# Kernel optimization log

Measured on AMD Instinct MI355X. Metric: run time of the kernel, lower is better.

## Reference

```python
import jax, jax.numpy as jnp
import numpy as np

START, STOP = 3, 4  # tag_to_ix['<START>'], tag_to_ix['<STOP>']
NEG = -10000.0


def _lstm_dir(x, w_ih, w_hh, b_ih, b_hh, h0, c0, reverse):
    # x: [S, E]; PyTorch gate order i, f, g, o
    H2 = h0.shape[0]
    xg = x @ w_ih.T + b_ih + b_hh  # [S, 4*H2] precompute input part

    def step(carry, xt):
        h, c = carry
        g = xt + h @ w_hh.T
        i, f, gg, o = jnp.split(g, 4)
        i, f, o = jax.nn.sigmoid(i), jax.nn.sigmoid(f), jax.nn.sigmoid(o)
        c = f * c + i * jnp.tanh(gg)
        h = o * jnp.tanh(c)
        return (h, c), h

    _, hs = jax.lax.scan(step, (h0, c0), xg, reverse=reverse)
    return hs  # [S, H2]


def setup_inputs() -> dict:
    key = jax.random.key(0)
    ks = jax.random.split(key, 16)
    S, E, H, T = 8192, 768, 1024, 5
    H2 = H // 2
    inp = {
        "embeddings": jax.random.normal(ks[0], (S, E), jnp.float32),
        "w_ih_f": jax.random.normal(ks[1], (4 * H2, E), jnp.float32) * 0.05,
        "w_hh_f": jax.random.normal(ks[2], (4 * H2, H2), jnp.float32) * 0.05,
        "b_ih_f": jax.random.normal(ks[3], (4 * H2,), jnp.float32) * 0.05,
        "b_hh_f": jax.random.normal(ks[4], (4 * H2,), jnp.float32) * 0.05,
        "w_ih_b": jax.random.normal(ks[5], (4 * H2, E), jnp.float32) * 0.05,
        "w_hh_b": jax.random.normal(ks[6], (4 * H2, H2), jnp.float32) * 0.05,
        "b_ih_b": jax.random.normal(ks[7], (4 * H2,), jnp.float32) * 0.05,
        "b_hh_b": jax.random.normal(ks[8], (4 * H2,), jnp.float32) * 0.05,
        "w_tag": jax.random.normal(ks[9], (T, H), jnp.float32) * 0.05,
        "b_tag": jax.random.normal(ks[10], (T,), jnp.float32) * 0.05,
        "h0_f": jax.random.normal(ks[12], (H2,), jnp.float32),
        "c0_f": jnp.zeros((H2,), jnp.float32),
        "h0_b": jax.random.normal(ks[13], (H2,), jnp.float32),
        "c0_b": jnp.zeros((H2,), jnp.float32),
    }
    trans = jax.random.normal(ks[11], (T, T), jnp.float32)
    trans = trans.at[START, :].set(NEG)  # never transition into START
    trans = trans.at[:, STOP].set(NEG)   # never transition out of STOP
    inp["transitions"] = trans
    return inp


def reference(embeddings, w_ih_f, w_hh_f, b_ih_f, b_hh_f,
              w_ih_b, w_hh_b, b_ih_b, b_hh_b,
              w_tag, b_tag, transitions, h0_f, c0_f, h0_b, c0_b):
    # BiLSTM features (batch=1, seq-major as in the torch module)
    h_f = _lstm_dir(embeddings, w_ih_f, w_hh_f, b_ih_f, b_hh_f, h0_f, c0_f, False)
    h_b = _lstm_dir(embeddings, w_ih_b, w_hh_b, b_ih_b, b_hh_b, h0_b, c0_b, True)
    lstm_out = jnp.concatenate([h_f, h_b], axis=-1)      # [S, H]
    feats = lstm_out @ w_tag.T + b_tag                   # [S, T]

    T = feats.shape[1]
    init = jnp.full((T,), NEG, feats.dtype).at[START].set(0.0)

    def vit_step(fv, feat):
        # m[next, prev] = fv[prev] + transitions[next, prev]
        m = fv[None, :] + transitions                     # [T, T]
        bp = jnp.argmax(m, axis=1)                        # [T] backpointers
        return jnp.max(m, axis=1) + feat, bp

    fv, bps = jax.lax.scan(vit_step, init, feats)         # bps: [S, T]
    terminal = fv + transitions[STOP]
    best = jnp.argmax(terminal)
    path_score = terminal[best]

    def back_step(tag, bp):
        return bp[tag], tag

    _, best_path = jax.lax.scan(back_step, best, bps, reverse=True)  # [S]
    return path_score, best_path
```

## Files before the change

### kernel.cpp

```cpp
#include <hip/hip_runtime.h>
#include <hip/hip_bf16.h>
#include <math.h>

#define DEV static __device__ __forceinline__

DEV float rl(float v, int i){ return __uint_as_float(__builtin_amdgcn_readlane(__float_as_uint(v), i)); }

typedef float f32x16 __attribute__((ext_vector_type(16)));

static constexpr size_t OFF_H     = 0;
static constexpr size_t OFF_FEATS = 33554432;
static constexpr size_t OFF_BPS   = OFF_FEATS + 163840;
static constexpr size_t OFF_FC    = OFF_BPS + 163840;
static constexpr size_t OFF_ECH   = OFF_FC + 5120;
static constexpr size_t OFF_EBEST = OFF_ECH + 1024;
static constexpr size_t OFF_HBUF  = OFF_EBEST + 256;
static constexpr size_t OFF_XG    = OFF_HBUF + 16384;
static constexpr size_t XG_BYTES  = 2ull*8192*2048*4;

__global__ __launch_bounds__(256) void xg_k(const float* __restrict__ emb,
                                            const float* __restrict__ wihf,
                                            const float* __restrict__ wihb,
                                            float* __restrict__ xg)
{
  const int tm = blockIdx.x * 128;
  const int tn = blockIdx.y * 128;
  const int tid = threadIdx.x;
  const int ty = tid >> 4, tx = tid & 15;
  __shared__ float As[16][132], Bs[16][132];
  float acc[8][8];
  #pragma unroll
  for (int i=0;i<8;i++)
    #pragma unroll
    for (int j=0;j<8;j++) acc[i][j] = 0.f;

  const int m  = tid & 127;
  const int n  = tn + m;
  const float* wih = (n & 2048) ? wihb : wihf;
  const float* arow = emb + (size_t)(tm+m)*768;
  const float* brow = wih + (size_t)(n&2047)*768;
  const int kq = (tid >> 7) << 2;

  for (int k0=0; k0<768; k0+=16){
    #pragma unroll
    for (int r=0;r<2;r++){
      const int kk = kq + r*8;
      float4 v = *reinterpret_cast<const float4*>(arow + k0 + kk);
      As[kk+0][m]=v.x; As[kk+1][m]=v.y; As[kk+2][m]=v.z; As[kk+3][m]=v.w;
      float4 u = *reinterpret_cast<const float4*>(brow + k0 + kk);
      Bs[kk+0][m]=u.x; Bs[kk+1][m]=u.y; Bs[kk+2][m]=u.z; Bs[kk+3][m]=u.w;
    }
    __syncthreads();
    #pragma unroll
    for (int k=0;k<16;k++){
      float4 a0 = *reinterpret_cast<const float4*>(&As[k][ty*8]);
      float4 a1 = *reinterpret_cast<const float4*>(&As[k][ty*8+4]);
      float4 b0 = *reinterpret_cast<const float4*>(&Bs[k][tx*8]);
      float4 b1 = *reinterpret_cast<const float4*>(&Bs[k][tx*8+4]);
      float af[8] = {a0.x,a0.y,a0.z,a0.w,a1.x,a1.y,a1.z,a1.w};
      float bf[8] = {b0.x,b0.y,b0.z,b0.w,b1.x,b1.y,b1.z,b1.w};
      #pragma unroll
      for (int i=0;i<8;i++)
        #pragma unroll
        for (int j=0;j<8;j++) acc[i][j] = fmaf(af[i], bf[j], acc[i][j]);
    }
    __syncthreads();
  }

  const int dd = tn >> 11;
  const int nb = tn & 2047;
  float* xgp = xg + (size_t)dd*8192*2048;
  #pragma unroll
  for (int i=0;i<8;i++){
    float* orow = xgp + (size_t)(tm+ty*8+i)*2048 + nb + tx*8;
    #pragma unroll
    for (int j=0;j<8;j+=4){
      float4 st = { acc[i][j], acc[i][j+1], acc[i][j+2], acc[i][j+3] };
      *reinterpret_cast<float4*>(orow + j) = st;
    }
  }
}

#define DOT16(X, OFF, W, B0, B1_, B2_, B3_) \
  _Pragma("unroll") for (int i=0;i<16;i+=4){ \
    B0 =fmaf(rl(X,OFF+i+0),W[i+0],B0 ); B1_=fmaf(rl(X,OFF+i+1),W[i+1],B1_); \
    B2_=fmaf(rl(X,OFF+i+2),W[i+2],B2_); B3_=fmaf(rl(X,OFF+i+3),W[i+3],B3_); }

__global__ __launch_bounds__(512,2) void lstm_xg(
    const float* __restrict__ whhf, const float* __restrict__ whhb,
    const float* __restrict__ bihf, const float* __restrict__ bhhf,
    const float* __restrict__ bihb, const float* __restrict__ bhhb,
    const float* __restrict__ h0f, const float* __restrict__ c0f,
    const float* __restrict__ h0b, const float* __restrict__ c0b,
    const float* __restrict__ xg,
    float* __restrict__ H, unsigned long long* __restrict__ hbuf)
{
  const int b  = blockIdx.x;
  const int d  = b >> 5;
  const int k  = b & 31;
  const int tid = threadIdx.x;
  const int w  = tid >> 6;
  const int l  = tid & 63;

  const float* whh = d ? whhb : whhf;
  const int grow = (l&3)*512 + k*16 + (l>>2);

  const float* pr = whh + (size_t)grow*512 + w*64;
  f32x16 wr0 = *reinterpret_cast<const f32x16*>(pr);
  f32x16 wr1 = *reinterpret_cast<const f32x16*>(pr+16);
  f32x16 wr2 = *reinterpret_cast<const f32x16*>(pr+32);
  f32x16 wr3 = *reinterpret_cast<const f32x16*>(pr+48);
  asm volatile("" : "+v"(wr0)); asm volatile("" : "+v"(wr1));
  asm volatile("" : "+v"(wr2)); asm volatile("" : "+v"(wr3));

  const float bias = (d?bihb:bihf)[grow] + (d?bhhb:bhhf)[grow];
  const float* xgp = xg + (size_t)d*8192*2048;

  const float* h0 = d ? h0b : h0f;
  float hv = h0[w*64 + l];
  float c  = (d?c0b:c0f)[k*16 + (l>>2)];

  __shared__ float part[2][8][64];

  float xq0 = 0.f, xq1 = 0.f;
  if (w==0){
    xq0 = xgp[(size_t)(d?8191:0)*2048 + grow];
    xq1 = xgp[(size_t)(d?8190:1)*2048 + grow];
  }

  for (int s=0; s<8192; s++){
    const int t  = d ? (8191-s) : s;
    const int pb = s & 1;
    float a0=0.f, a1=0.f, a2=0.f, a3=0.f;
    DOT16(hv, 0, wr0, a0,a1,a2,a3)
    DOT16(hv,16, wr1, a0,a1,a2,a3)
    DOT16(hv,32, wr2, a0,a1,a2,a3)
    DOT16(hv,48, wr3, a0,a1,a2,a3)
    part[pb][w][l] = (a0+a1)+(a2+a3);
    __syncthreads();

    if (w==0){
      float r = ((part[pb][0][l]+part[pb][1][l])+(part[pb][2][l]+part[pb][3][l]))
              + ((part[pb][4][l]+part[pb][5][l])+(part[pb][6][l]+part[pb][7][l]))
              + bias + xq0;
      const bool isg = ((l&3)==2);
      float xx = isg ? 2.f*r : r;
      float sg = 1.f/(1.f + expf(-xx));
      float a  = isg ? fmaf(2.f,sg,-1.f) : sg;
      const int lb = l & ~3;
      float ig = __shfl(a, lb);
      float fg = __shfl(a, lb+1);
      float gg = __shfl(a, lb+2);
      float og = __shfl(a, lb+3);
      if ((l&3)==0){
        c = fmaf(fg, c, ig*gg);
        float h = og * tanhf(c);
        const int unit = k*16 + (l>>2);
        unsigned long long pk = ((unsigned long long)(unsigned)(s+1) << 32)
                              | (unsigned long long)__float_as_uint(h);
        __hip_atomic_store(hbuf + (pb<<10) + d*512 + unit, pk,
                           __ATOMIC_RELAXED, __HIP_MEMORY_SCOPE_AGENT);
        H[(size_t)t*1024 + d*512 + unit] = h;
      }
      xq0 = xq1;
      if (s<8190) xq1 = xgp[(size_t)(d?(8189-s):(s+2))*2048 + grow];
    }

    if (s<8191){
      const unsigned long long* hp = hbuf + (pb<<10) + d*512 + w*64 + l;
      const unsigned want = (unsigned)(s+1);
      unsigned long long p0 = __hip_atomic_load(hp, __ATOMIC_RELAXED, __HIP_MEMORY_SCOPE_AGENT);
      while ((unsigned)(p0>>32) < want){
        __builtin_amdgcn_s_sleep(1);
        p0 = __hip_atomic_load(hp, __ATOMIC_RELAXED, __HIP_MEMORY_SCOPE_AGENT);
      }
      hv = __uint_as_float((unsigned)p0);
    }
  }
}

__global__ __launch_bounds__(512,2) void lstm_legacy(
    const float* __restrict__ emb,
    const float* __restrict__ whhf, const float* __restrict__ whhb,
    const float* __restrict__ wihf, const float* __restrict__ wihb,
    const float* __restrict__ bihf, const float* __restrict__ bhhf,
    const float* __restrict__ bihb, const float* __restrict__ bhhb,
    const float* __restrict__ h0f, const float* __restrict__ c0f,
    const float* __restrict__ h0b, const float* __restrict__ c0b,
    float* __restrict__ H, unsigned long long* __restrict__ hbuf)
{
  const int b  = blockIdx.x;
  const int d  = b >> 5;
  const int k  = b & 31;
  const int tid = threadIdx.x;
  const int w  = tid >> 6;
  const int l  = tid & 63;

  const float* whh = d ? whhb : whhf;
  const float* wih = d ? wihb : wihf;
  const int grow = (l&3)*512 + k*16 + (l>>2);

  const float* pr = whh + (size_t)grow*512 + w*64;
  f32x16 wr0 = *reinterpret_cast<const f32x16*>(pr);
  f32x16 wr1 = *reinterpret_cast<const f32x16*>(pr+16);
  f32x16 wr2 = *reinterpret_cast<const f32x16*>(pr+32);
  f32x16 wr3 = *reinterpret_cast<const f32x16*>(pr+48);
  const float* pi = wih + (size_t)grow*768 + w*96;
  f32x16 wi0 = *reinterpret_cast<const f32x16*>(pi);
  f32x16 wi1 = *reinterpret_cast<const f32x16*>(pi+16);
  f32x16 wi2 = *reinterpret_cast<const f32x16*>(pi+32);
  f32x16 wi3 = *reinterpret_cast<const f32x16*>(pi+48);
  f32x16 wi4 = *reinterpret_cast<const f32x16*>(pi+64);
  f32x16 wi5 = *reinterpret_cast<const f32x16*>(pi+80);
  asm volatile("" : "+v"(wr0)); asm volatile("" : "+v"(wr1));
  asm volatile("" : "+v"(wr2)); asm volatile("" : "+v"(wr3));
  asm volatile("" : "+v"(wi0)); asm volatile("" : "+v"(wi1));
  asm volatile("" : "+v"(wi2)); asm volatile("" : "+v"(wi3));
  asm volatile("" : "+v"(wi4)); asm volatile("" : "+v"(wi5));

  const float bias = (d?bihb:bihf)[grow] + (d?bhhb:bhhf)[grow];
  const float* h0 = d ? h0b : h0f;
  float hv = h0[w*64 + l];
  float c  = (d?c0b:c0f)[k*16 + (l>>2)];

  __shared__ float part[2][8][64];

#define EPART(X0,X1,B0,B1_,B2_,B3_) \
  DOT16(X0, 0, wi0, B0,B1_,B2_,B3_) DOT16(X0,16, wi1, B0,B1_,B2_,B3_) \
  DOT16(X0,32, wi2, B0,B1_,B2_,B3_) DOT16(X0,48, wi3, B0,B1_,B2_,B3_) \
  DOT16(X1, 0, wi4, B0,B1_,B2_,B3_) DOT16(X1,16, wi5, B0,B1_,B2_,B3_)

  float acc_e;
  {
    const int tA = d ? 8191 : 0;
    const float* e = emb + (size_t)tA*768 + w*96 + l;
    float x0 = e[0];
    float x1 = (l<32) ? e[64] : 0.f;
    float b0=0.f,b1=0.f,b2=0.f,b3=0.f;
    EPART(x0,x1,b0,b1,b2,b3);
    acc_e = (b0+b1)+(b2+b3);
  }
  float ev0, ev1;
  {
    const int tB = d ? 8190 : 1;
    const float* e = emb + (size_t)tB*768 + w*96 + l;
    ev0 = e[0];
    ev1 = (l<32) ? e[64] : 0.f;
  }

  for (int s=0; s<8192; s++){
    const int t  = d ? (8191-s) : s;
    const int pb = s & 1;
    float a0=acc_e, a1=0.f, a2=0.f, a3=0.f;
    DOT16(hv, 0, wr0, a0,a1,a2,a3)
    DOT16(hv,16, wr1, a0,a1,a2,a3)
    DOT16(hv,32, wr2, a0,a1,a2,a3)
    DOT16(hv,48, wr3, a0,a1,a2,a3)
    part[pb][w][l] = (a0+a1)+(a2+a3);
    __syncthreads();

    if (w==0){
      float r = ((part[pb][0][l]+part[pb][1][l])+(part[pb][2][l]+part[pb][3][l]))
              + ((part[pb][4][l]+part[pb][5][l])+(part[pb][6][l]+part[pb][7][l])) + bias;
      const bool isg = ((l&3)==2);
      float xx = isg ? 2.f*r : r;
      float sg = 1.f/(1.f + expf(-xx));
      float a  = isg ? fmaf(2.f,sg,-1.f) : sg;
      const int lb = l & ~3;
      float ig = __shfl(a, lb);
      float fg = __shfl(a, lb+1);
      float gg = __shfl(a, lb+2);
      float og = __shfl(a, lb+3);
      if ((l&3)==0){
        c = fmaf(fg, c, ig*gg);
        float h = og * tanhf(c);
        const int unit = k*16 + (l>>2);
        unsigned long long pk = ((unsigned long long)(unsigned)(s+1) << 32)
                              | (unsigned long long)__float_as_uint(h);
        __hip_atomic_store(hbuf + (pb<<10) + d*512 + unit, pk,
                           __ATOMIC_RELAXED, __HIP_MEMORY_SCOPE_AGENT);
        H[(size_t)t*1024 + d*512 + unit] = h;
      }
    }

    if (s<8191){
      float nx0=0.f, nx1=0.f;
      if (s<8190){
        const int t2 = d ? (8189-s) : (s+2);
        const float* e = emb + (size_t)t2*768 + w*96 + l;
        nx0 = e[0];
        nx1 = (l<32) ? e[64] : 0.f;
      }
      float b0=0.f,b1=0.f,b2=0.f,b3=0.f;
      EPART(ev0,ev1,b0,b1,b2,b3);
      acc_e = (b0+b1)+(b2+b3);
      ev0=nx0; ev1=nx1;

      const unsigned long long* hp = hbuf + (pb<<10) + d*512 + w*64 + l;
      const unsigned want = (unsigned)(s+1);
      unsigned long long p0 = __hip_atomic_load(hp, __ATOMIC_RELAXED, __HIP_MEMORY_SCOPE_AGENT);
      while ((unsigned)(p0>>32) < want){
        __builtin_amdgcn_s_sleep(1);
        p0 = __hip_atomic_load(hp, __ATOMIC_RELAXED, __HIP_MEMORY_SCOPE_AGENT);
      }
      hv = __uint_as_float((unsigned)p0);
    }
  }
#undef EPART
}

__global__ void feats_k(const float* __restrict__ H, const float* __restrict__ wtag,
                        const float* __restrict__ btag, float* __restrict__ feats)
{
  const int r = blockIdx.x*4 + (threadIdx.x>>6);
  const int l = threadIdx.x & 63;
  const float* hrow = H + (size_t)r*1024;
  float hv[16];
  #pragma unroll
  for (int j=0;j<16;j++) hv[j] = hrow[j*64 + l];
  #pragma unroll
  for (int n=0;n<5;n++){
    const float* wrow = wtag + n*1024;
    float acc = 0.f;
    #pragma unroll
    for (int j=0;j<16;j++) acc = fmaf(hv[j], wrow[j*64+l], acc);
    #pragma unroll
    for (int off=32; off; off>>=1) acc += __shfl_xor(acc, off);
    if (l==0) feats[r*5+n] = acc + btag[n];
  }
}

__global__ void vit_fv(const float* __restrict__ feats, const float* __restrict__ trans,
                       int* __restrict__ bps, float* __restrict__ out, int* __restrict__ ebest)
{
  const int l = threadIdx.x & 63;
  const bool active = (l < 25);
  const int n = l/5;
  float tr0=0,tr1=0,tr2=0,tr3=0,tr4=0;
  if (active){ tr0=trans[n*5+0]; tr1=trans[n*5+1]; tr2=trans[n*5+2]; tr3=trans[n*5+3]; tr4=trans[n*5+4]; }
  const float NEG = -10000.0f;
  float fv0=NEG, fv1=NEG, fv2=NEG, fv3=0.f, fv4=NEG;

  float ring[16];
  #pragma unroll
  for (int j=0;j<16;j++) ring[j] = active ? feats[j*5+n] : 0.f;

  for (int tb=0; tb<8192; tb+=16){
    #pragma unroll
    for (int j=0;j<16;j++){
      const int t = tb + j;
      float ft = ring[j];
      float m = fv0 + tr0; int a = 0; float v;
      v = fv1 + tr1; if (v > m){ m=v; a=1; }
      v = fv2 + tr2; if (v > m){ m=v; a=2; }
      v = fv3 + tr3; if (v > m){ m=v; a=3; }
      v = fv4 + tr4; if (v > m){ m=v; a=4; }
      float fnew = m + ft;
      if (active && (l%5)==0) bps[t*5+n] = a;
      fv0 = __shfl(fnew, 0);  fv1 = __shfl(fnew, 5);  fv2 = __shfl(fnew, 10);
      fv3 = __shfl(fnew, 15); fv4 = __shfl(fnew, 20);
      const int tf = t + 16;
      ring[j] = (active && tf < 8192) ? feats[tf*5+n] : 0.f;
    }
  }
  if (l==0){
    float t0=trans[20], t1=trans[21], t2=trans[22], t3=trans[23], t4=trans[24];
    float m = fv0 + t0; int a = 0; float v;
    v = fv1 + t1; if (v > m){ m=v; a=1; }
    v = fv2 + t2; if (v > m){ m=v; a=2; }
    v = fv3 + t3; if (v > m){ m=v; a=3; }
    v = fv4 + t4; if (v > m){ m=v; a=4; }
    out[0] = m;
    ebest[0] = a;
  }
}

__global__ void bt_maps(const int* __restrict__ bps, int* __restrict__ Fc)
{
  __shared__ int sm[160];
  const int c = blockIdx.x, tid = threadIdx.x;
  for (int idx=tid; idx<160; idx+=64) sm[idx] = bps[c*160+idx];
  __syncthreads();
  if (tid<5){
    int cur = tid;
    for (int j=31;j>=0;j--) cur = sm[j*5+cur];
    Fc[c*5+tid] = cur;
  }
}

__global__ void bt_seq(const int* __restrict__ Fc, const int* __restrict__ ebest,
                       int* __restrict__ echunk)
{
  __shared__ int sm[1280];
  const int tid = threadIdx.x;
  for (int idx=tid; idx<1280; idx+=64) sm[idx]=Fc[idx];
  __syncthreads();
  if (tid==0){
    int e = ebest[0];
    for (int c=255;c>=0;c--){ echunk[c]=e; e = sm[c*5+e]; }
  }
}

__global__ void bt_emit(const int* __restrict__ bps, const int* __restrict__ echunk,
                        float* __restrict__ out)
{
  __shared__ int sm[160];
  const int c=blockIdx.x, tid=threadIdx.x;
  for (int idx=tid; idx<160; idx+=64) sm[idx]=bps[c*160+idx];
  __syncthreads();
  if (tid==0){
    int tag = echunk[c];
    out[1 + c*32 + 31] = (float)tag;
    for (int j=31;j>=1;j--){ tag = sm[j*5+tag]; out[1 + c*32 + j-1] = (float)tag; }
  }
}

extern "C" void kernel_launch(void* const* d_in, const int* in_sizes, int n_in,
                              void* d_out, int out_size, void* d_ws, size_t ws_size,
                              hipStream_t stream)
{
  (void)in_sizes; (void)n_in; (void)out_size;
  const float* emb  = (const float*)d_in[0];
  const float* wihf = (const float*)d_in[1];
  const float* whhf = (const float*)d_in[2];
  const float* bihf = (const float*)d_in[3];
  const float* bhhf = (const float*)d_in[4];
  const float* wihb = (const float*)d_in[5];
  const float* whhb = (const float*)d_in[6];
  const float* bihb = (const float*)d_in[7];
  const float* bhhb = (const float*)d_in[8];
  const float* wtag = (const float*)d_in[9];
  const float* btag = (const float*)d_in[10];
  const float* h0f  = (const float*)d_in[11];
  const float* c0f  = (const float*)d_in[12];
  const float* h0b  = (const float*)d_in[13];
  const float* c0b  = (const float*)d_in[14];
  const float* trans= (const float*)d_in[15];
  float* out = (float*)d_out;

  char* ws = (char*)d_ws;
  float* H      = (float*)(ws + OFF_H);
  float* feats  = (float*)(ws + OFF_FEATS);
  int*   bps    = (int*)  (ws + OFF_BPS);
  int*   Fc     = (int*)  (ws + OFF_FC);
  int*   echunk = (int*)  (ws + OFF_ECH);
  int*   ebest  = (int*)  (ws + OFF_EBEST);
  unsigned long long* hbuf = (unsigned long long*)(ws + OFF_HBUF);
  float* xg     = (float*)(ws + OFF_XG);

  hipMemsetAsync(hbuf, 0, 2*1024*8, stream);

  const bool use_xg = ws_size >= OFF_XG + XG_BYTES;
  if (use_xg){
    xg_k<<<dim3(64,32), 256, 0, stream>>>(emb, wihf, wihb, xg);
    lstm_xg<<<64, 512, 0, stream>>>(whhf, whhb, bihf, bhhf, bihb, bhhb,
                                    h0f, c0f, h0b, c0b, xg, H, hbuf);
  } else {
    lstm_legacy<<<64, 512, 0, stream>>>(emb, whhf, whhb, wihf, wihb,
                                        bihf, bhhf, bihb, bhhb,
                                        h0f, c0f, h0b, c0b, H, hbuf);
  }
  feats_k<<<2048, 256, 0, stream>>>(H, wtag, btag, feats);
  vit_fv<<<1, 64, 0, stream>>>(feats, trans, bps, out, ebest);
  bt_maps<<<256, 64, 0, stream>>>(bps, Fc);
  bt_seq<<<1, 64, 0, stream>>>(Fc, ebest, echunk);
  bt_emit<<<256, 64, 0, stream>>>(bps, echunk, out);
}
```

Baseline: 13.83 ms.

## Fuse input-projection GEMM into persistent LSTM kernel with per-row readiness flags

Replaces the separate xg GEMM launch and LSTM launch with one kernel. Blocks 0-63 run the recurrent LSTM, and the other 192 blocks compute xg tiles in time order from both sequence ends, bumping a per-row counter when each tile is done. LSTM blocks spin on that counter before reading each new 128-row block, so the recurrence can start before the whole GEMM has finished. The aim is to hide the GEMM behind the serial recurrence. The cost is co-residency assumptions for the spin-waits, atomic tile stores, and a tweaked spin-wait backoff in the hidden-state exchange.

Measured after the change: 13.46 ms. 2.7% less time.

```diff
diff --git a/kernel.cpp b/kernel.cpp
--- a/kernel.cpp
+++ b/kernel.cpp
@@ -7,6 +7,7 @@
 DEV float rl(float v, int i){ return __uint_as_float(__builtin_amdgcn_readlane(__float_as_uint(v), i)); }
 
 typedef float f32x16 __attribute__((ext_vector_type(16)));
+typedef unsigned long long u64;
 
 static constexpr size_t OFF_H     = 0;
 static constexpr size_t OFF_FEATS = 33554432;
@@ -14,20 +15,23 @@
 static constexpr size_t OFF_FC    = OFF_BPS + 163840;
 static constexpr size_t OFF_ECH   = OFF_FC + 5120;
 static constexpr size_t OFF_EBEST = OFF_ECH + 1024;
-static constexpr size_t OFF_HBUF  = OFF_EBEST + 256;
+static constexpr size_t OFF_RC    = OFF_EBEST + 256;
+static constexpr size_t OFF_HBUF  = OFF_RC + 256;
 static constexpr size_t OFF_XG    = OFF_HBUF + 16384;
 static constexpr size_t XG_BYTES  = 2ull*8192*2048*4;
 
-__global__ __launch_bounds__(256) void xg_k(const float* __restrict__ emb,
-                                            const float* __restrict__ wihf,
-                                            const float* __restrict__ wihb,
-                                            float* __restrict__ xg)
-{
-  const int tm = blockIdx.x * 128;
-  const int tn = blockIdx.y * 128;
-  const int tid = threadIdx.x;
+#define DOT16(X, OFF, W, B0, B1_, B2_, B3_) \
+  _Pragma("unroll") for (int i=0;i<16;i+=4){ \
+    B0 =fmaf(rl(X,OFF+i+0),W[i+0],B0 ); B1_=fmaf(rl(X,OFF+i+1),W[i+1],B1_); \
+    B2_=fmaf(rl(X,OFF+i+2),W[i+2],B2_); B3_=fmaf(rl(X,OFF+i+3),W[i+3],B3_); }
+
+DEV void xg_tile(const float* __restrict__ emb, const float* __restrict__ wihf,
+                 const float* __restrict__ wihb, float* __restrict__ xg,
+                 int* rowcnt, int tm32, int tn32, bool doflag,
+                 float (*As)[132], float (*Bs)[132], int tid)
+{
+  const int tmb = tm32*128, tnb = tn32*128;
   const int ty = tid >> 4, tx = tid & 15;
-  __shared__ float As[16][132], Bs[16][132];
   float acc[8][8];
   #pragma unroll
   for (int i=0;i<8;i++)
@@ -35,9 +39,9 @@
     for (int j=0;j<8;j++) acc[i][j] = 0.f;
 
   const int m  = tid & 127;
-  const int n  = tn + m;
+  const int n  = tnb + m;
   const float* wih = (n & 2048) ? wihb : wihf;
-  const float* arow = emb + (size_t)(tm+m)*768;
+  const float* arow = emb + (size_t)(tmb+m)*768;
   const float* brow = wih + (size_t)(n&2047)*768;
   const int kq = (tid >> 7) << 2;
 
@@ -52,11 +56,11 @@
     }
     __syncthreads();
     #pragma unroll
-    for (int k=0;k<16;k++){
-      float4 a0 = *reinterpret_cast<const float4*>(&As[k][ty*8]);
-      float4 a1 = *reinterpret_cast<const float4*>(&As[k][ty*8+4]);
-      float4 b0 = *reinterpret_cast<const float4*>(&Bs[k][tx*8]);
-      float4 b1 = *reinterpret_cast<const float4*>(&Bs[k][tx*8+4]);
+    for (int kk2=0;kk2<16;kk2++){
+      float4 a0 = *reinterpret_cast<const float4*>(&As[kk2][ty*8]);
+      float4 a1 = *reinterpret_cast<const float4*>(&As[kk2][ty*8+4]);
+      float4 b0 = *reinterpret_cast<const float4*>(&Bs[kk2][tx*8]);
+      float4 b1 = *reinterpret_cast<const float4*>(&Bs[kk2][tx*8+4]);
       float af[8] = {a0.x,a0.y,a0.z,a0.w,a1.x,a1.y,a1.z,a1.w};
       float bf[8] = {b0.x,b0.y,b0.z,b0.w,b1.x,b1.y,b1.z,b1.w};
       #pragma unroll
@@ -67,35 +71,62 @@
     __syncthreads();
   }
 
-  const int dd = tn >> 11;
-  const int nb = tn & 2047;
+  const int dd = tnb >> 11, nb = tnb & 2047;
   float* xgp = xg + (size_t)dd*8192*2048;
   #pragma unroll
   for (int i=0;i<8;i++){
-    float* orow = xgp + (size_t)(tm+ty*8+i)*2048 + nb + tx*8;
-    #pragma unroll
-    for (int j=0;j<8;j+=4){
-      float4 st = { acc[i][j], acc[i][j+1], acc[i][j+2], acc[i][j+3] };
-      *reinterpret_cast<float4*>(orow + j) = st;
-    }
-  }
-}
-
-#define DOT16(X, OFF, W, B0, B1_, B2_, B3_) \
-  _Pragma("unroll") for (int i=0;i<16;i+=4){ \
-    B0 =fmaf(rl(X,OFF+i+0),W[i+0],B0 ); B1_=fmaf(rl(X,OFF+i+1),W[i+1],B1_); \
-    B2_=fmaf(rl(X,OFF+i+2),W[i+2],B2_); B3_=fmaf(rl(X,OFF+i+3),W[i+3],B3_); }
-
-__global__ __launch_bounds__(512,2) void lstm_xg(
+    float* orow = xgp + (size_t)(tmb+ty*8+i)*2048 + nb + tx*8;
+    #pragma unroll
+    for (int j=0;j<8;j+=2){
+      u64 uu = ((u64)__float_as_uint(acc[i][j+1])<<32) | (u64)__float_as_uint(acc[i][j]);
+      __hip_atomic_store(reinterpret_cast<u64*>(orow + j), uu,
+                         __ATOMIC_RELAXED, __HIP_MEMORY_SCOPE_AGENT);
+    }
+  }
+  __syncthreads();
+  if (doflag && tid==0)
+    __hip_atomic_fetch_add(rowcnt + tm32, 1, __ATOMIC_RELAXED, __HIP_MEMORY_SCOPE_AGENT);
+}
+
+DEV void wait_row(const int* rc, int tm){
+  while (__hip_atomic_load(rc + tm, __ATOMIC_RELAXED, __HIP_MEMORY_SCOPE_AGENT) < 32)
+    __builtin_amdgcn_s_sleep(8);
+  __builtin_amdgcn_sched_barrier(0);
+  asm volatile("" ::: "memory");
+}
+
+__global__ __launch_bounds__(512,2) void fused_k(
+    const float* __restrict__ emb,
+    const float* __restrict__ wihf, const float* __restrict__ wihb,
     const float* __restrict__ whhf, const float* __restrict__ whhb,
     const float* __restrict__ bihf, const float* __restrict__ bhhf,
     const float* __restrict__ bihb, const float* __restrict__ bhhb,
     const float* __restrict__ h0f, const float* __restrict__ c0f,
     const float* __restrict__ h0b, const float* __restrict__ c0b,
-    const float* __restrict__ xg,
-    float* __restrict__ H, unsigned long long* __restrict__ hbuf)
-{
-  const int b  = blockIdx.x;
+    float* __restrict__ xg, float* __restrict__ H,
+    u64* __restrict__ hbuf, int* __restrict__ rowcnt)
+{
+  __shared__ float smemf[8448];
+  const int b = blockIdx.x;
+
+  if (b >= 64){
+    const int tid = threadIdx.x & 255;
+    const int sb  = threadIdx.x >> 8;
+    float (*As)[132] = (float(*)[132])(smemf + sb*4224);
+    float (*Bs)[132] = (float(*)[132])(smemf + sb*4224 + 2112);
+    const int wkr = (b - 64)*2 + sb;
+    for (int r=0; r<6; r++){
+      int j = wkr + r*384;
+      const bool real = (j < 2048);
+      if (!real) j = 2047;
+      const int p = j >> 5, tn32 = j & 31;
+      const int tm32 = (p & 1) ? (63 - (p>>1)) : (p>>1);
+      xg_tile(emb, wihf, wihb, xg, rowcnt, tm32, tn32, real, As, Bs, tid);
+    }
+    return;
+  }
+
+  float (*part)[8][64] = (float(*)[8][64])smemf;
   const int d  = b >> 5;
   const int k  = b & 31;
   const int tid = threadIdx.x;
@@ -110,8 +141,6 @@
   f32x16 wr1 = *reinterpret_cast<const f32x16*>(pr+16);
   f32x16 wr2 = *reinterpret_cast<const f32x16*>(pr+32);
   f32x16 wr3 = *reinterpret_cast<const f32x16*>(pr+48);
-  asm volatile("" : "+v"(wr0)); asm volatile("" : "+v"(wr1));
-  asm volatile("" : "+v"(wr2)); asm volatile("" : "+v"(wr3));
 
   const float bias = (d?bihb:bihf)[grow] + (d?bhhb:bhhf)[grow];
   const float* xgp = xg + (size_t)d*8192*2048;
@@ -120,10 +149,9 @@
   float hv = h0[w*64 + l];
   float c  = (d?c0b:c0f)[k*16 + (l>>2)];
 
-  __shared__ float part[2][8][64];
-
   float xq0 = 0.f, xq1 = 0.f;
   if (w==0){
+    wait_row(rowcnt, d ? 63 : 0);
     xq0 = xgp[(size_t)(d?8191:0)*2048 + grow];
     xq1 = xgp[(size_t)(d?8190:1)*2048 + grow];
   }
@@ -156,22 +184,26 @@
         c = fmaf(fg, c, ig*gg);
         float h = og * tanhf(c);
         const int unit = k*16 + (l>>2);
-        unsigned long long pk = ((unsigned long long)(unsigned)(s+1) << 32)
-                              | (unsigned long long)__float_as_uint(h);
+        u64 pk = ((u64)(unsigned)(s+1) << 32) | (u64)__float_as_uint(h);
         __hip_atomic_store(hbuf + (pb<<10) + d*512 + unit, pk,
                            __ATOMIC_RELAXED, __HIP_MEMORY_SCOPE_AGENT);
         H[(size_t)t*1024 + d*512 + unit] = h;
       }
       xq0 = xq1;
-      if (s<8190) xq1 = xgp[(size_t)(d?(8189-s):(s+2))*2048 + grow];
+      if (s<8190){
+        const int t2 = d ? (8189-s) : (s+2);
+        if (d==0 ? ((t2 & 127)==0) : ((t2 & 127)==127)) wait_row(rowcnt, t2>>7);
+        xq1 = xgp[(size_t)t2*2048 + grow];
+      }
     }
 
     if (s<8191){
-      const unsigned long long* hp = hbuf + (pb<<10) + d*512 + w*64 + l;
+      const u64* hp = hbuf + (pb<<10) + d*512 + w*64 + l;
       const unsigned want = (unsigned)(s+1);
-      unsigned long long p0 = __hip_atomic_load(hp, __ATOMIC_RELAXED, __HIP_MEMORY_SCOPE_AGENT);
+      u64 p0 = __hip_atomic_load(hp, __ATOMIC_RELAXED, __HIP_MEMORY_SCOPE_AGENT);
+      int it = 0;
       while ((unsigned)(p0>>32) < want){
-        __builtin_amdgcn_s_sleep(1);
+        if (++it > 4) __builtin_amdgcn_s_sleep(1);
         p0 = __hip_atomic_load(hp, __ATOMIC_RELAXED, __HIP_MEMORY_SCOPE_AGENT);
       }
       hv = __uint_as_float((unsigned)p0);
@@ -187,7 +219,7 @@
     const float* __restrict__ bihb, const float* __restrict__ bhhb,
     const float* __restrict__ h0f, const float* __restrict__ c0f,
     const float* __restrict__ h0b, const float* __restrict__ c0b,
-    float* __restrict__ H, unsigned long long* __restrict__ hbuf)
+    float* __restrict__ H, u64* __restrict__ hbuf)
 {
   const int b  = blockIdx.x;
   const int d  = b >> 5;
@@ -212,11 +244,6 @@
   f32x16 wi3 = *reinterpret_cast<const f32x16*>(pi+48);
   f32x16 wi4 = *reinterpret_cast<const f32x16*>(pi+64);
   f32x16 wi5 = *reinterpret_cast<const f32x16*>(pi+80);
-  asm volatile("" : "+v"(wr0)); asm volatile("" : "+v"(wr1));
-  asm volatile("" : "+v"(wr2)); asm volatile("" : "+v"(wr3));
-  asm volatile("" : "+v"(wi0)); asm volatile("" : "+v"(wi1));
-  asm volatile("" : "+v"(wi2)); asm volatile("" : "+v"(wi3));
-  asm volatile("" : "+v"(wi4)); asm volatile("" : "+v"(wi5));
 
   const float bias = (d?bihb:bihf)[grow] + (d?bhhb:bhhf)[grow];
   const float* h0 = d ? h0b : h0f;
@@ -275,8 +302,7 @@
         c = fmaf(fg, c, ig*gg);
         float h = og * tanhf(c);
         const int unit = k*16 + (l>>2);
-        unsigned long long pk = ((unsigned long long)(unsigned)(s+1) << 32)
-                              | (unsigned long long)__float_as_uint(h);
+        u64 pk = ((u64)(unsigned)(s+1) << 32) | (u64)__float_as_uint(h);
         __hip_atomic_store(hbuf + (pb<<10) + d*512 + unit, pk,
                            __ATOMIC_RELAXED, __HIP_MEMORY_SCOPE_AGENT);
         H[(size_t)t*1024 + d*512 + unit] = h;
@@ -296,9 +322,9 @@
       acc_e = (b0+b1)+(b2+b3);
       ev0=nx0; ev1=nx1;
 
-      const unsigned long long* hp = hbuf + (pb<<10) + d*512 + w*64 + l;
+      const u64* hp = hbuf + (pb<<10) + d*512 + w*64 + l;
       const unsigned want = (unsigned)(s+1);
-      unsigned long long p0 = __hip_atomic_load(hp, __ATOMIC_RELAXED, __HIP_MEMORY_SCOPE_AGENT);
+      u64 p0 = __hip_atomic_load(hp, __ATOMIC_RELAXED, __HIP_MEMORY_SCOPE_AGENT);
       while ((unsigned)(p0>>32) < want){
         __builtin_amdgcn_s_sleep(1);
         p0 = __hip_atomic_load(hp, __ATOMIC_RELAXED, __HIP_MEMORY_SCOPE_AGENT);
@@ -445,16 +471,17 @@
   int*   Fc     = (int*)  (ws + OFF_FC);
   int*   echunk = (int*)  (ws + OFF_ECH);
   int*   ebest  = (int*)  (ws + OFF_EBEST);
-  unsigned long long* hbuf = (unsigned long long*)(ws + OFF_HBUF);
+  int*   rowcnt = (int*)  (ws + OFF_RC);
+  u64*   hbuf   = (u64*)  (ws + OFF_HBUF);
   float* xg     = (float*)(ws + OFF_XG);
 
-  hipMemsetAsync(hbuf, 0, 2*1024*8, stream);
+  hipMemsetAsync(rowcnt, 0, 256 + 16384, stream);
 
   const bool use_xg = ws_size >= OFF_XG + XG_BYTES;
   if (use_xg){
-    xg_k<<<dim3(64,32), 256, 0, stream>>>(emb, wihf, wihb, xg);
-    lstm_xg<<<64, 512, 0, stream>>>(whhf, whhb, bihf, bhhf, bihb, bhhb,
-                                    h0f, c0f, h0b, c0b, xg, H, hbuf);
+    fused_k<<<256, 512, 0, stream>>>(emb, wihf, wihb, whhf, whhb,
+                                     bihf, bhhf, bihb, bhhb,
+                                     h0f, c0f, h0b, c0b, xg, H, hbuf, rowcnt);
   } else {
     lstm_legacy<<<64, 512, 0, stream>>>(emb, whhf, whhb, wihf, wihb,
                                         bihf, bhhf, bihb, bhhb,
```
